# Optimization experiments

Hardware: AMD Instinct MI355X
Metric: run time of the kernel (lower is better)

Reference implementation:

```python
import jax, jax.numpy as jnp
import numpy as np

N_NODES = 100000
N_EDGES = 1600000
D_IN = 128
D_HID = 128
D_OUT = 128
E_DIM = 16


def setup_inputs() -> dict:
    key = jax.random.key(0)
    ks = jax.random.split(key, 8)
    nh = jax.random.normal(ks[0], (N_NODES, D_IN), dtype=jnp.float32)
    eh = jax.random.normal(ks[1], (N_EDGES, E_DIM), dtype=jnp.float32)
    edge_index = jax.random.randint(ks[2], (2, N_EDGES), 0, N_NODES, dtype=jnp.int64)
    # 2-layer MLP params (Linear -> relu -> Linear), Kaiming-ish init
    W1 = jax.random.normal(ks[3], (D_IN, D_HID), dtype=jnp.float32) / np.sqrt(D_IN)
    b1 = jnp.zeros((D_HID,), dtype=jnp.float32)
    W2 = jax.random.normal(ks[4], (D_HID, D_OUT), dtype=jnp.float32) / np.sqrt(D_HID)
    b2 = jnp.zeros((D_OUT,), dtype=jnp.float32)
    return {"nh": nh, "eh": eh, "edge_index": edge_index,
            "W1": W1, "b1": b1, "W2": W2, "b2": b2}


def reference(nh, eh, edge_index, W1, b1, W2, b2):
    src, dst = edge_index[0], edge_index[1]
    n = nh.shape[0]
    # degree of destination nodes via scatter_add of ones
    deg = jax.ops.segment_sum(jnp.ones(dst.shape[0], dtype=nh.dtype), dst,
                              num_segments=n)
    # deg^{-1/2} with inf -> 0 for isolated nodes
    deg_inv_sqrt = jnp.where(deg > 0, jax.lax.rsqrt(jnp.maximum(deg, 1e-30)),
                             jnp.zeros_like(deg))
    # gather source features, scale by deg_inv_sqrt[src]  -> [E, d]
    n_msg = nh[src] * deg_inv_sqrt[src][:, None]
    # scatter_add messages to destinations  -> [N, d]
    agg = jax.ops.segment_sum(n_msg, dst, num_segments=n)
    agg = agg * deg_inv_sqrt[:, None]
    # 2-layer MLP (nf_lin): Linear -> relu -> Linear
    h = jax.nn.relu(agg @ W1 + b1)
    n_h = h @ W2 + b2
    return (n_h, eh)
```

## Files before the change

kernel.cpp:

```cpp
#include <hip/hip_runtime.h>
#include <hip/hip_bf16.h>

#define NNODES 100000
#define NEDGES 1600000
#define DIM 128
#define EDIM 16

#define NBKT 256
#define BW 391
#define CHUNK 4096
#define EPT 16
#define NCHUNK ((NEDGES + CHUNK - 1) / CHUNK)

#define O_BH     0u
#define O_BOFS   4096u
#define O_BTAIL  8192u
#define O_W1P    16384u
#define O_W2P    49152u
#define O_RP     81920u
#define O_DINV   491520u
#define O_CSR    921600u
#define O_EBUF   7340032u

typedef __attribute__((ext_vector_type(8))) short bf16x8;
typedef __attribute__((ext_vector_type(4))) float f32x4;

__device__ __forceinline__ unsigned rn_bf16(float x) {
    unsigned u = __float_as_uint(x);
    return (u + 0x7FFFu + ((u >> 16) & 1u)) >> 16;
}

__global__ __launch_bounds__(256) void bhist(const int* __restrict__ dst,
                                             int* __restrict__ bh) {
    __shared__ int s[NBKT];
    s[threadIdx.x] = 0;
    __syncthreads();
    for (int e = blockIdx.x * 256 + threadIdx.x; e < NEDGES; e += gridDim.x * 256)
        atomicAdd(&s[dst[e] / BW], 1);
    __syncthreads();
    atomicAdd(&bh[threadIdx.x], s[threadIdx.x]);
}

__global__ __launch_bounds__(256) void bscan(const int* __restrict__ bh,
                                             int* __restrict__ bofs,
                                             int* __restrict__ btail) {
    __shared__ int s[256];
    const int t = threadIdx.x;
    int v = bh[t];
    s[t] = v;
    __syncthreads();
    for (int off = 1; off < 256; off <<= 1) {
        int x = (t >= off) ? s[t - off] : 0;
        __syncthreads();
        s[t] += x;
        __syncthreads();
    }
    int ex = s[t] - v;
    bofs[t] = ex;
    btail[t] = ex;
    if (t == 255) bofs[256] = s[255];
}

__global__ __launch_bounds__(256) void bscatter(const int* __restrict__ src,
                                                const int* __restrict__ dst,
                                                int* __restrict__ btail,
                                                unsigned* __restrict__ ebuf) {
    __shared__ int lcnt[NBKT], lofs[NBKT], lcur[NBKT], gbase[NBKT];
    __shared__ unsigned obuf[CHUNK];
    __shared__ unsigned char qb[CHUNK];
    const int tid = threadIdx.x;
    const int e0 = blockIdx.x * CHUNK;
    const int n = min(CHUNK, NEDGES - e0);

    lcnt[tid] = 0;
    __syncthreads();

    int myb[EPT];
    unsigned myrec[EPT];
#pragma unroll
    for (int k = 0; k < EPT; ++k) {
        int q = k * 256 + tid;
        if (q < n) {
            int e = e0 + q;
            int d = dst[e];
            int bb = d / BW;
            int dl = d - bb * BW;
            myrec[k] = (unsigned)src[e] | ((unsigned)dl << 17);
            myb[k] = bb;
            atomicAdd(&lcnt[bb], 1);
        } else myb[k] = -1;
    }
    __syncthreads();

    const int c = lcnt[tid];
    lofs[tid] = c;
    __syncthreads();
    for (int off = 1; off < 256; off <<= 1) {
        int x = (tid >= off) ? lofs[tid - off] : 0;
        __syncthreads();
        lofs[tid] += x;
        __syncthreads();
    }
    int ex = lofs[tid] - c;
    lofs[tid] = ex;
    lcur[tid] = ex;
    gbase[tid] = atomicAdd(&btail[tid], c);
    __syncthreads();

#pragma unroll
    for (int k = 0; k < EPT; ++k) {
        if (myb[k] >= 0) {
            int p = atomicAdd(&lcur[myb[k]], 1);
            obuf[p] = myrec[k];
            qb[p] = (unsigned char)myb[k];
        }
    }
    __syncthreads();

    for (int q = tid; q < n; q += 256) {
        int bb = qb[q];
        ebuf[gbase[bb] + (q - lofs[bb])] = obuf[q];
    }
}

__global__ __launch_bounds__(256) void csr_build(const unsigned* __restrict__ ebuf,
                                                 const int* __restrict__ bofs,
                                                 int* __restrict__ rp,
                                                 float* __restrict__ dinv,
                                                 int* __restrict__ csr) {
    __shared__ int fcnt[392];
    __shared__ int fcur[392];
    __shared__ int part[49];
    const int b = blockIdx.x, tid = threadIdx.x;
    const int nodebase = b * BW;
    const int nn = min(BW, NNODES - nodebase);
    const int e0 = bofs[b], e1 = bofs[b + 1];

    for (int i = tid; i < 392; i += 256) fcnt[i] = 0;
    __syncthreads();
    for (int q = e0 + tid; q < e1; q += 256)
        atomicAdd(&fcnt[ebuf[q] >> 17], 1);
    __syncthreads();

    if (tid < 49) {
        int s = 0;
#pragma unroll
        for (int k = 0; k < 8; ++k) {
            int idx = 8 * tid + k;
            if (idx < 392) s += fcnt[idx];
        }
        part[tid] = s;
    }
    __syncthreads();
    if (tid == 0) {
        int s = 0;
        for (int k = 0; k < 49; ++k) { int v = part[k]; part[k] = s; s += v; }
    }
    __syncthreads();
    if (tid < 49) {
        int s = part[tid];
#pragma unroll
        for (int k = 0; k < 8; ++k) {
            int idx = 8 * tid + k;
            if (idx < 392) { int v = fcnt[idx]; fcnt[idx] = s; s += v; }
        }
    }
    __syncthreads();

    for (int i = tid; i < nn; i += 256) {
        int deg = fcnt[i + 1] - fcnt[i];
        rp[nodebase + i] = e0 + fcnt[i];
        dinv[nodebase + i] = (deg > 0) ? rsqrtf((float)deg) : 0.0f;
        fcur[i] = fcnt[i];
    }
    if (b == NBKT - 1 && tid == 0) rp[NNODES] = NEDGES;
    __syncthreads();

    for (int q = e0 + tid; q < e1; q += 256) {
        unsigned rec = ebuf[q];
        int dl = rec >> 17;
        int pos = atomicAdd(&fcur[dl], 1);
        csr[e0 + pos] = (int)(rec & 0x1FFFFu);
    }
}

__global__ __launch_bounds__(256) void wpack_kernel(const float* __restrict__ W1,
                                                    const float* __restrict__ W2,
                                                    ushort* __restrict__ w1p,
                                                    ushort* __restrict__ w2p) {
    int idx = blockIdx.x * 256 + threadIdx.x;
    int i = idx & 7;
    int l = (idx >> 3) & 63;
    int c = (idx >> 9) & 7;
    int t = (idx >> 12) & 3;
    int k = 32 * t + 8 * (l >> 4) + i;
    int j = 16 * c + (l & 15);
    w1p[idx] = (ushort)rn_bf16(W1[k * DIM + j]);
    w2p[idx] = (ushort)rn_bf16(W2[k * DIM + j]);
}

__global__ __launch_bounds__(256) void agg_kernel(const int* __restrict__ rp,
                                                  const int* __restrict__ csr,
                                                  const float* __restrict__ dinv,
                                                  const float* __restrict__ nh,
                                                  float* __restrict__ agg) {
    const int lane = threadIdx.x & 63;
    const int half = lane >> 5;
    const int l32  = lane & 31;
    const int wid     = (blockIdx.x * 256 + threadIdx.x) >> 6;
    const int nwaves  = (gridDim.x * 256) >> 6;

    for (int n = wid; n < NNODES; n += nwaves) {
        const int beg = rp[n];
        const int end = rp[n + 1];
        const float dn = dinv[n];
        float ax = 0.0f, ay = 0.0f, az = 0.0f, aw = 0.0f;
        int i = beg;
        for (; i + 8 <= end; i += 8) {
            int s0 = csr[i + 0 + half];
            int s1 = csr[i + 2 + half];
            int s2 = csr[i + 4 + half];
            int s3 = csr[i + 6 + half];
            float w0 = dinv[s0], w1 = dinv[s1], w2 = dinv[s2], w3 = dinv[s3];
            float4 f0 = ((const float4*)(nh + (size_t)s0 * DIM))[l32];
            float4 f1 = ((const float4*)(nh + (size_t)s1 * DIM))[l32];
            float4 f2 = ((const float4*)(nh + (size_t)s2 * DIM))[l32];
            float4 f3 = ((const float4*)(nh + (size_t)s3 * DIM))[l32];
            ax = fmaf(f0.x, w0, ax); ay = fmaf(f0.y, w0, ay);
            az = fmaf(f0.z, w0, az); aw = fmaf(f0.w, w0, aw);
            ax = fmaf(f1.x, w1, ax); ay = fmaf(f1.y, w1, ay);
            az = fmaf(f1.z, w1, az); aw = fmaf(f1.w, w1, aw);
            ax = fmaf(f2.x, w2, ax); ay = fmaf(f2.y, w2, ay);
            az = fmaf(f2.z, w2, az); aw = fmaf(f2.w, w2, aw);
            ax = fmaf(f3.x, w3, ax); ay = fmaf(f3.y, w3, ay);
            az = fmaf(f3.z, w3, az); aw = fmaf(f3.w, w3, aw);
        }
        for (; i + 2 <= end; i += 2) {
            int s0 = csr[i + half];
            float w0 = dinv[s0];
            float4 f0 = ((const float4*)(nh + (size_t)s0 * DIM))[l32];
            ax = fmaf(f0.x, w0, ax); ay = fmaf(f0.y, w0, ay);
            az = fmaf(f0.z, w0, az); aw = fmaf(f0.w, w0, aw);
        }
        if (i < end) {
            int s0 = csr[i];
            float w0 = half ? 0.0f : dinv[s0];
            float4 f0 = ((const float4*)(nh + (size_t)s0 * DIM))[l32];
            ax = fmaf(f0.x, w0, ax); ay = fmaf(f0.y, w0, ay);
            az = fmaf(f0.z, w0, az); aw = fmaf(f0.w, w0, aw);
        }
        ax += __shfl_xor(ax, 32);
        ay += __shfl_xor(ay, 32);
        az += __shfl_xor(az, 32);
        aw += __shfl_xor(aw, 32);
        if (half == 0) {
            ((float4*)(agg + (size_t)n * DIM))[l32] =
                make_float4(ax * dn, ay * dn, az * dn, aw * dn);
        }
    }
}

__global__ __launch_bounds__(512) void mlp_mfma(const float* __restrict__ x,
                                                const ushort* __restrict__ w1p,
                                                const ushort* __restrict__ w2p,
                                                const float* __restrict__ b1,
                                                const float* __restrict__ b2,
                                                float* __restrict__ out) {
    __shared__ __align__(16) ushort sW[2][16384];
    __shared__ __align__(16) float  sH[8][2048];

    const int tid  = threadIdx.x;
    const int lane = tid & 63;
    const int w    = tid >> 6;
    const int m    = lane & 15;
    const int g    = lane >> 4;

    {
        const float4* s1 = (const float4*)w1p;
        const float4* s2 = (const float4*)w2p;
        float4* d1 = (float4*)sW[0];
        float4* d2 = (float4*)sW[1];
        for (int q = tid; q < 2048; q += 512) d1[q] = s1[q];
        for (int q = tid; q < 2048; q += 512) d2[q] = s2[q];
    }

    float bias1[8], bias2[8];
#pragma unroll
    for (int c = 0; c < 8; ++c) { bias1[c] = b1[16 * c + m]; bias2[c] = b2[16 * c + m]; }

    __syncthreads();

    const int rowbase = blockIdx.x * 128 + w * 16;
    char* hbase = (char*)sH[w];
    const int node = rowbase + m;
    const bool valid = (node < NNODES);

    f32x4 acc[8];
#pragma unroll
    for (int c = 0; c < 8; ++c) acc[c] = f32x4{0.f, 0.f, 0.f, 0.f};

#pragma unroll
    for (int t = 0; t < 4; ++t) {
        const int kb = 32 * t + 8 * g;
        float4 xa = make_float4(0.f, 0.f, 0.f, 0.f);
        float4 xb = make_float4(0.f, 0.f, 0.f, 0.f);
        if (valid) {
            const float4* px = (const float4*)(x + (size_t)node * DIM + kb);
            xa = px[0];
            xb = px[1];
        }
        float v[8] = {xa.x, xa.y, xa.z, xa.w, xb.x, xb.y, xb.z, xb.w};
        bf16x8 ahi, alo;
#pragma unroll
        for (int i = 0; i < 8; ++i) {
            unsigned hu = rn_bf16(v[i]);
            float hf = __uint_as_float(hu << 16);
            ahi[i] = (short)hu;
            alo[i] = (short)rn_bf16(v[i] - hf);
        }
#pragma unroll
        for (int c = 0; c < 8; ++c) {
            bf16x8 bw = *(const bf16x8*)&sW[0][((t * 8 + c) * 64 + lane) * 8];
            acc[c] = __builtin_amdgcn_mfma_f32_16x16x32_bf16(alo, bw, acc[c], 0, 0, 0);
            acc[c] = __builtin_amdgcn_mfma_f32_16x16x32_bf16(ahi, bw, acc[c], 0, 0, 0);
        }
    }

#pragma unroll
    for (int c = 0; c < 8; ++c) {
#pragma unroll
        for (int r = 0; r < 4; ++r) {
            int row = 4 * g + r;
            float hv = fmaxf(acc[c][r] + bias1[c], 0.0f);
            int off = (row * 512 + (16 * c + m) * 4) ^ ((row & 7) << 4);
            *(float*)(hbase + off) = hv;
        }
    }

#pragma unroll
    for (int c = 0; c < 8; ++c) acc[c] = f32x4{0.f, 0.f, 0.f, 0.f};

#pragma unroll
    for (int t = 0; t < 4; ++t) {
        const int kb = 32 * t + 8 * g;
        int o0 = (m * 512 + kb * 4) ^ ((m & 7) << 4);
        int o1 = (m * 512 + kb * 4 + 16) ^ ((m & 7) << 4);
        f32x4 va = *(const f32x4*)(hbase + o0);
        f32x4 vb = *(const f32x4*)(hbase + o1);
        float v[8] = {va[0], va[1], va[2], va[3], vb[0], vb[1], vb[2], vb[3]};
        bf16x8 ahi, alo;
#pragma unroll
        for (int i = 0; i < 8; ++i) {
            unsigned hu = rn_bf16(v[i]);
            float hf = __uint_as_float(hu << 16);
            ahi[i] = (short)hu;
            alo[i] = (short)rn_bf16(v[i] - hf);
        }
#pragma unroll
        for (int c = 0; c < 8; ++c) {
            bf16x8 bw = *(const bf16x8*)&sW[1][((t * 8 + c) * 64 + lane) * 8];
            acc[c] = __builtin_amdgcn_mfma_f32_16x16x32_bf16(alo, bw, acc[c], 0, 0, 0);
            acc[c] = __builtin_amdgcn_mfma_f32_16x16x32_bf16(ahi, bw, acc[c], 0, 0, 0);
        }
    }

#pragma unroll
    for (int c = 0; c < 8; ++c) {
#pragma unroll
        for (int r = 0; r < 4; ++r) {
            int row = 4 * g + r;
            int off = (row * 512 + (16 * c + m) * 4) ^ ((row & 7) << 4);
            *(float*)(hbase + off) = acc[c][r] + bias2[c];
        }
    }

#pragma unroll
    for (int it = 0; it < 8; ++it) {
        int row = 2 * it + (lane >> 5);
        int c4  = lane & 31;
        int off = (row * 512 + c4 * 16) ^ ((row & 7) << 4);
        f32x4 val = *(const f32x4*)(hbase + off);
        int nodeS = rowbase + row;
        if (nodeS < NNODES)
            *(f32x4*)(out + (size_t)nodeS * DIM + (size_t)c4 * 4) = val;
    }
}

extern "C" void kernel_launch(void* const* d_in, const int* in_sizes, int n_in,
                              void* d_out, int out_size, void* d_ws, size_t ws_size,
                              hipStream_t stream) {
    const float* nh = (const float*)d_in[0];
    const float* eh = (const float*)d_in[1];
    const int*   ei = (const int*)d_in[2];
    const float* W1 = (const float*)d_in[3];
    const float* b1 = (const float*)d_in[4];
    const float* W2 = (const float*)d_in[5];
    const float* b2 = (const float*)d_in[6];

    char* ws = (char*)d_ws;
    int*      bh    = (int*)(ws + O_BH);
    int*      bofs  = (int*)(ws + O_BOFS);
    int*      btail = (int*)(ws + O_BTAIL);
    ushort*   w1p   = (ushort*)(ws + O_W1P);
    ushort*   w2p   = (ushort*)(ws + O_W2P);
    int*      rp    = (int*)(ws + O_RP);
    float*    dinv  = (float*)(ws + O_DINV);
    int*      csr   = (int*)(ws + O_CSR);
    unsigned* ebuf  = (unsigned*)(ws + O_EBUF);

    float* out_nh = (float*)d_out;
    float* out_eh = out_nh + (size_t)NNODES * DIM;

    const int* src = ei;
    const int* dst = ei + NEDGES;

    hipMemsetAsync(bh, 0, NBKT * sizeof(int), stream);

    bhist<<<256, 256, 0, stream>>>(dst, bh);
    bscan<<<1, 256, 0, stream>>>(bh, bofs, btail);
    wpack_kernel<<<64, 256, 0, stream>>>(W1, W2, w1p, w2p);
    bscatter<<<NCHUNK, 256, 0, stream>>>(src, dst, btail, ebuf);
    csr_build<<<NBKT, 256, 0, stream>>>(ebuf, bofs, rp, dinv, csr);
    agg_kernel<<<4096, 256, 0, stream>>>(rp, csr, dinv, nh, out_nh);
    mlp_mfma<<<(NNODES + 127) / 128, 512, 0, stream>>>(out_nh, w1p, w2p, b1, b2, out_nh);

    hipMemcpyAsync(out_eh, eh, (size_t)NEDGES * EDIM * sizeof(float),
                   hipMemcpyDeviceToDevice, stream);
}
```

Measured before the change: 466.7 us.

## Fuse eh copy into aggregation kernel and prefetch CSR indices

```diff
diff --git a/kernel.cpp b/kernel.cpp
--- a/kernel.cpp
+++ b/kernel.cpp
@@ -11,6 +11,9 @@
 #define CHUNK 4096
 #define EPT 16
 #define NCHUNK ((NEDGES + CHUNK - 1) / CHUNK)
+
+#define AGG_BLKS 4096
+#define CPY_BLKS 1024
 
 #define O_BH     0u
 #define O_BOFS   4096u
@@ -203,52 +206,66 @@
                                                   const int* __restrict__ csr,
                                                   const float* __restrict__ dinv,
                                                   const float* __restrict__ nh,
-                                                  float* __restrict__ agg) {
+                                                  float* __restrict__ agg,
+                                                  const float* __restrict__ eh,
+                                                  float* __restrict__ out_eh) {
+    if (blockIdx.x >= AGG_BLKS) {
+        const float4* s = (const float4*)eh;
+        float4* d = (float4*)out_eh;
+        const int total = NEDGES * EDIM / 4;
+        for (int q = (blockIdx.x - AGG_BLKS) * 256 + threadIdx.x; q < total;
+             q += CPY_BLKS * 256)
+            d[q] = s[q];
+        return;
+    }
+
     const int lane = threadIdx.x & 63;
     const int half = lane >> 5;
     const int l32  = lane & 31;
     const int wid     = (blockIdx.x * 256 + threadIdx.x) >> 6;
-    const int nwaves  = (gridDim.x * 256) >> 6;
+    const int nwaves  = (AGG_BLKS * 256) >> 6;
 
     for (int n = wid; n < NNODES; n += nwaves) {
         const int beg = rp[n];
         const int end = rp[n + 1];
         const float dn = dinv[n];
         float ax = 0.0f, ay = 0.0f, az = 0.0f, aw = 0.0f;
-        int i = beg;
-        for (; i + 8 <= end; i += 8) {
-            int s0 = csr[i + 0 + half];
-            int s1 = csr[i + 2 + half];
-            int s2 = csr[i + 4 + half];
-            int s3 = csr[i + 6 + half];
-            float w0 = dinv[s0], w1 = dinv[s1], w2 = dinv[s2], w3 = dinv[s3];
-            float4 f0 = ((const float4*)(nh + (size_t)s0 * DIM))[l32];
-            float4 f1 = ((const float4*)(nh + (size_t)s1 * DIM))[l32];
-            float4 f2 = ((const float4*)(nh + (size_t)s2 * DIM))[l32];
-            float4 f3 = ((const float4*)(nh + (size_t)s3 * DIM))[l32];
-            ax = fmaf(f0.x, w0, ax); ay = fmaf(f0.y, w0, ay);
-            az = fmaf(f0.z, w0, az); aw = fmaf(f0.w, w0, aw);
-            ax = fmaf(f1.x, w1, ax); ay = fmaf(f1.y, w1, ay);
-            az = fmaf(f1.z, w1, az); aw = fmaf(f1.w, w1, aw);
-            ax = fmaf(f2.x, w2, ax); ay = fmaf(f2.y, w2, ay);
-            az = fmaf(f2.z, w2, az); aw = fmaf(f2.w, w2, aw);
-            ax = fmaf(f3.x, w3, ax); ay = fmaf(f3.y, w3, ay);
-            az = fmaf(f3.z, w3, az); aw = fmaf(f3.w, w3, aw);
-        }
-        for (; i + 2 <= end; i += 2) {
-            int s0 = csr[i + half];
-            float w0 = dinv[s0];
-            float4 f0 = ((const float4*)(nh + (size_t)s0 * DIM))[l32];
-            ax = fmaf(f0.x, w0, ax); ay = fmaf(f0.y, w0, ay);
-            az = fmaf(f0.z, w0, az); aw = fmaf(f0.w, w0, aw);
-        }
-        if (i < end) {
-            int s0 = csr[i];
-            float w0 = half ? 0.0f : dinv[s0];
-            float4 f0 = ((const float4*)(nh + (size_t)s0 * DIM))[l32];
-            ax = fmaf(f0.x, w0, ax); ay = fmaf(f0.y, w0, ay);
-            az = fmaf(f0.z, w0, az); aw = fmaf(f0.w, w0, aw);
-        }
+
+        if (beg < end) {
+            const int last = end - 1;
+            int c0 = csr[min(beg + 0 + half, last)];
+            int c1 = csr[min(beg + 2 + half, last)];
+            int c2 = csr[min(beg + 4 + half, last)];
+            int c3 = csr[min(beg + 6 + half, last)];
+            for (int i = beg; i < end; i += 8) {
+                const int inext = i + 8;
+                int p0 = c0, p1 = c1, p2 = c2, p3 = c3;
+                if (inext < end) {
+                    p0 = csr[min(inext + 0 + half, last)];
+                    p1 = csr[min(inext + 2 + half, last)];
+                    p2 = csr[min(inext + 4 + half, last)];
+                    p3 = csr[min(inext + 6 + half, last)];
+                }
+                float w0 = (i + 0 + half < end) ? dinv[c0] : 0.0f;
+                float w1 = (i + 2 + half < end) ? dinv[c1] : 0.0f;
+                float w2 = (i + 4 + half < end) ? dinv[c2] : 0.0f;
+                float w3 = (i + 6 + half < end) ? dinv[c3] : 0.0f;
+                float4 f0 = ((const float4*)(nh + (size_t)c0 * DIM))[l32];
+                float4 f1 = ((const float4*)(nh + (size_t)c1 * DIM))[l32];
+                float4 f2 = ((const float4*)(nh + (size_t)c2 * DIM))[l32];
+                float4 f3 = ((const float4*)(nh + (size_t)c3 * DIM))[l32];
+                ax = fmaf(f0.x, w0, ax); ay = fmaf(f0.y, w0, ay);
+                az = fmaf(f0.z, w0, az); aw = fmaf(f0.w, w0, aw);
+                ax = fmaf(f1.x, w1, ax); ay = fmaf(f1.y, w1, ay);
+                az = fmaf(f1.z, w1, az); aw = fmaf(f1.w, w1, aw);
+                ax = fmaf(f2.x, w2, ax); ay = fmaf(f2.y, w2, ay);
+                az = fmaf(f2.z, w2, az); aw = fmaf(f2.w, w2, aw);
+                ax = fmaf(f3.x, w3, ax); ay = fmaf(f3.y, w3, ay);
+                az = fmaf(f3.z, w3, az); aw = fmaf(f3.w, w3, aw);
+                c0 = p0; c1 = p1; c2 = p2; c3 = p3;
+            }
+        }
+
         ax += __shfl_xor(ax, 32);
         ay += __shfl_xor(ay, 32);
         az += __shfl_xor(az, 32);
@@ -421,9 +438,7 @@
     wpack_kernel<<<64, 256, 0, stream>>>(W1, W2, w1p, w2p);
     bscatter<<<NCHUNK, 256, 0, stream>>>(src, dst, btail, ebuf);
     csr_build<<<NBKT, 256, 0, stream>>>(ebuf, bofs, rp, dinv, csr);
-    agg_kernel<<<4096, 256, 0, stream>>>(rp, csr, dinv, nh, out_nh);
+    agg_kernel<<<AGG_BLKS + CPY_BLKS, 256, 0, stream>>>(rp, csr, dinv, nh, out_nh,
+                                                        eh, out_eh);
     mlp_mfma<<<(NNODES + 127) / 128, 512, 0, stream>>>(out_nh, w1p, w2p, b1, b2, out_nh);
-
-    hipMemcpyAsync(out_eh, eh, (size_t)NEDGES * EDIM * sizeof(float),
-                   hipMemcpyDeviceToDevice, stream);
-}
+}
```

After: 468.8 us. Within noise of the previous version (+0.4%).
